# Performance work log

Measured on AMD Instinct MI355X. Metric: run time of the kernel, lower is better.

## Reference

```python
import jax, jax.numpy as jnp
import numpy as np

NIN = 128
NOUT = 128


def setup_inputs() -> dict:
    key = jax.random.key(0)
    k_adj, k_node, k_wi, k_wj = jax.random.split(key, 4)
    B, N = 4, 256
    adj = jax.random.uniform(k_adj, (B, 1, N, N), dtype=jnp.float32)
    node = jax.random.normal(k_node, (B, NIN, N), dtype=jnp.float32)
    # 1x1 conv weights, stored as [nout, nin] (squeezed from [nout, nin, 1, 1])
    scale = 1.0 / np.sqrt(NIN)
    Wi = jax.random.normal(k_wi, (NOUT, NIN), dtype=jnp.float32) * scale
    Wj = jax.random.normal(k_wj, (NOUT, NIN), dtype=jnp.float32) * scale
    return {"adj": adj, "node": node, "Wi": Wi, "Wj": Wj}


def reference(adj, node, Wi, Wj):
    # adj: [B,1,N,N], node: [B,nin,N]
    N = adj.shape[-1]
    # broadcast node across rows and mask by adjacency: [B,nin,N,N]
    x = node[:, :, None, :] * adj
    # 1x1 convs == channel contractions
    yi = jnp.einsum('oc,bcij->boij', Wi, x)
    yj = jnp.einsum('oc,bcij->boij', Wj, x)
    I = jnp.eye(N, dtype=x.dtype)
    return I * yi + (1.0 - I) * yj
```

## Files before the change

kernel.cpp:

```cpp
#include <hip/hip_runtime.h>

#define NIN  128
#define NOUT 128
#define NN   256
#define BB   4

__global__ __launch_bounds__(256) void precompute_u(
    const float* __restrict__ node,
    const float* __restrict__ Wi,
    const float* __restrict__ Wj,
    float* __restrict__ ui,
    float* __restrict__ uj)
{
    const int bo = blockIdx.x;
    const int b  = bo >> 7;
    const int o  = bo & (NOUT - 1);
    const int t  = threadIdx.x;

    const float* np_ = node + (size_t)b * NIN * NN + t;
    const float* wi  = Wi + o * NIN;
    const float* wj  = Wj + o * NIN;

    float ai = 0.f, aj = 0.f;
    #pragma unroll 16
    for (int c = 0; c < NIN; ++c) {
        const float n = np_[c * NN];
        ai = fmaf(wi[c], n, ai);
        aj = fmaf(wj[c], n, aj);
    }
    ui[bo * NN + t] = ai;
    uj[bo * NN + t] = aj;
}

__global__ __launch_bounds__(256) void stream_out(
    const float* __restrict__ adj,
    const float* __restrict__ ui,
    const float* __restrict__ uj,
    float* __restrict__ out)
{
    const int blk = blockIdx.x;
    const int bo  = blk >> 3;
    const int rc  = blk & 7;
    const int b   = bo >> 7;
    const int t   = threadIdx.x;
    const int jb  = (t & 63) << 2;
    const int rr  = t >> 6;

    const float4 vj   = *(const float4*)&uj[bo * NN + jb];
    const float* uip  = ui + bo * NN;
    const float* adjb = adj + (size_t)b * (NN * NN);
    float*       outp = out + (size_t)bo * (NN * NN);

    const int i0 = (rc << 5) + rr;
    #pragma unroll
    for (int r = 0; r < 8; ++r) {
        const int i = i0 + (r << 2);
        const float s_ii = uip[i];
        const float4 a = *(const float4*)&adjb[i * NN + jb];
        float4 v;
        v.x = (i == jb + 0) ? s_ii : vj.x;
        v.y = (i == jb + 1) ? s_ii : vj.y;
        v.z = (i == jb + 2) ? s_ii : vj.z;
        v.w = (i == jb + 3) ? s_ii : vj.w;
        float4 rs;
        rs.x = a.x * v.x;
        rs.y = a.y * v.y;
        rs.z = a.z * v.z;
        rs.w = a.w * v.w;
        *(float4*)&outp[i * NN + jb] = rs;
    }
}

__global__ __launch_bounds__(256) void nodeconv_fused(
    const float* __restrict__ adj, const float* __restrict__ node,
    const float* __restrict__ Wi, const float* __restrict__ Wj,
    float* __restrict__ out)
{
    __shared__ float si[NN];
    __shared__ float sj[NN];
    const int bo = blockIdx.x;
    const int b  = bo >> 7;
    const int o  = bo & (NOUT - 1);
    const int t  = threadIdx.x;
    {
        const float* np_ = node + (size_t)(b * NIN) * NN + t;
        const float* wi  = Wi + o * NIN;
        const float* wj  = Wj + o * NIN;
        float ai = 0.f, aj = 0.f;
        #pragma unroll 8
        for (int c = 0; c < NIN; ++c) {
            const float n = np_[(size_t)c * NN];
            ai += wi[c] * n;
            aj += wj[c] * n;
        }
        si[t] = ai;
        sj[t] = aj;
    }
    __syncthreads();
    const int jb   = (t & 63) << 2;
    const int rrow = t >> 6;
    const float4 vj = *(const float4*)&sj[jb];
    const float* adjb = adj + (size_t)b * (NN * NN);
    float*       outp = out + (size_t)bo * (NN * NN);
    #pragma unroll 4
    for (int r = 0; r < 64; ++r) {
        const int i = (r << 2) + rrow;
        const float s_ii = si[i];
        const float4 a = *(const float4*)&adjb[i * NN + jb];
        float4 v;
        v.x = (i == jb + 0) ? s_ii : vj.x;
        v.y = (i == jb + 1) ? s_ii : vj.y;
        v.z = (i == jb + 2) ? s_ii : vj.z;
        v.w = (i == jb + 3) ? s_ii : vj.w;
        float4 rs;
        rs.x = a.x * v.x; rs.y = a.y * v.y; rs.z = a.z * v.z; rs.w = a.w * v.w;
        *(float4*)&outp[i * NN + jb] = rs;
    }
}

extern "C" void kernel_launch(void* const* d_in, const int* in_sizes, int n_in,
                              void* d_out, int out_size, void* d_ws, size_t ws_size,
                              hipStream_t stream) {
    const float* adj  = (const float*)d_in[0];
    const float* node = (const float*)d_in[1];
    const float* Wi   = (const float*)d_in[2];
    const float* Wj   = (const float*)d_in[3];
    float* out = (float*)d_out;

    const size_t u_elems = (size_t)BB * NOUT * NN;
    const size_t need    = 2 * u_elems * sizeof(float);

    if (ws_size >= need) {
        float* ui = (float*)d_ws;
        float* uj = ui + u_elems;
        precompute_u<<<dim3(BB * NOUT), dim3(256), 0, stream>>>(node, Wi, Wj, ui, uj);
        stream_out<<<dim3(BB * NOUT * 8), dim3(256), 0, stream>>>(adj, ui, uj, out);
    } else {
        nodeconv_fused<<<dim3(BB * NOUT), dim3(256), 0, stream>>>(adj, node, Wi, Wj, out);
    }
}
```

Measured before the change: 147.9 us.

## Reuse adjacency tile across output-channel group and use nontemporal stores

The streaming kernel now loads a 16-row adjacency tile into registers once and reuses it for 8 output channels, instead of reloading adj for every output channel. Stores switch to nontemporal builtins so the large output write stream bypasses cache retention. This cuts adjacency read traffic, which was mostly served by L2 anyway. The cost is fewer blocks (1024 vs 4096), each doing more work, and a different block-to-memory mapping.

```diff
diff --git a/kernel.cpp b/kernel.cpp
--- a/kernel.cpp
+++ b/kernel.cpp
@@ -4,6 +4,8 @@
 #define NOUT 128
 #define NN   256
 #define BB   4
+
+typedef float v4f __attribute__((ext_vector_type(4)));
 
 __global__ __launch_bounds__(256) void precompute_u(
     const float* __restrict__ node,
@@ -32,42 +34,54 @@
     uj[bo * NN + t] = aj;
 }
 
-__global__ __launch_bounds__(256) void stream_out(
+#define OG 8
+#define RCH 16
+
+__global__ __launch_bounds__(256) void stream_out_og(
     const float* __restrict__ adj,
     const float* __restrict__ ui,
     const float* __restrict__ uj,
     float* __restrict__ out)
 {
     const int blk = blockIdx.x;
-    const int bo  = blk >> 3;
-    const int rc  = blk & 7;
-    const int b   = bo >> 7;
-    const int t   = threadIdx.x;
-    const int jb  = (t & 63) << 2;
-    const int rr  = t >> 6;
+    const int og  = blk & 15;
+    const int rc  = (blk >> 4) & 15;
+    const int b   = blk >> 8;
 
-    const float4 vj   = *(const float4*)&uj[bo * NN + jb];
-    const float* uip  = ui + bo * NN;
+    const int t  = threadIdx.x;
+    const int jb = (t & 63) << 2;
+    const int rr = t >> 6;
+
     const float* adjb = adj + (size_t)b * (NN * NN);
-    float*       outp = out + (size_t)bo * (NN * NN);
 
-    const int i0 = (rc << 5) + rr;
+    v4f a[4];
     #pragma unroll
-    for (int r = 0; r < 8; ++r) {
-        const int i = i0 + (r << 2);
-        const float s_ii = uip[i];
-        const float4 a = *(const float4*)&adjb[i * NN + jb];
-        float4 v;
-        v.x = (i == jb + 0) ? s_ii : vj.x;
-        v.y = (i == jb + 1) ? s_ii : vj.y;
-        v.z = (i == jb + 2) ? s_ii : vj.z;
-        v.w = (i == jb + 3) ? s_ii : vj.w;
-        float4 rs;
-        rs.x = a.x * v.x;
-        rs.y = a.y * v.y;
-        rs.z = a.z * v.z;
-        rs.w = a.w * v.w;
-        *(float4*)&outp[i * NN + jb] = rs;
+    for (int r = 0; r < 4; ++r) {
+        const int i = (rc << 4) + rr + (r << 2);
+        a[r] = *(const v4f*)&adjb[i * NN + jb];
+    }
+
+    const int obase = b * NOUT + og * OG;
+
+    #pragma unroll 2
+    for (int o = 0; o < OG; ++o) {
+        const int bo = obase + o;
+        const v4f   vj  = *(const v4f*)&uj[bo * NN + jb];
+        const float* uip = ui + bo * NN;
+        float*       outp = out + (size_t)bo * (NN * NN);
+
+        #pragma unroll
+        for (int r = 0; r < 4; ++r) {
+            const int i = (rc << 4) + rr + (r << 2);
+            const float s_ii = uip[i];
+            v4f v;
+            v.x = (i == jb + 0) ? s_ii : vj.x;
+            v.y = (i == jb + 1) ? s_ii : vj.y;
+            v.z = (i == jb + 2) ? s_ii : vj.z;
+            v.w = (i == jb + 3) ? s_ii : vj.w;
+            const v4f rs = a[r] * v;
+            __builtin_nontemporal_store(rs, (v4f*)&outp[i * NN + jb]);
+        }
     }
 }
 
@@ -134,7 +148,7 @@
         float* ui = (float*)d_ws;
         float* uj = ui + u_elems;
         precompute_u<<<dim3(BB * NOUT), dim3(256), 0, stream>>>(node, Wi, Wj, ui, uj);
-        stream_out<<<dim3(BB * NOUT * 8), dim3(256), 0, stream>>>(adj, ui, uj, out);
+        stream_out_og<<<dim3(BB * (NOUT / OG) * (NN / RCH)), dim3(256), 0, stream>>>(adj, ui, uj, out);
     } else {
         nodeconv_fused<<<dim3(BB * NOUT), dim3(256), 0, stream>>>(adj, node, Wi, Wj, out);
     }
```

After: 152.0 us. 2.8% more time.

## Fuse projection and streaming into one kernel with row chunks and nontemporal stores

Applied to the files above, without the earlier changes.

Replaces the two-kernel path (precompute projections into workspace, then stream output) with a single kernel. Each block recomputes the per-(batch, out-channel) projections into shared memory and then writes a quarter of the output rows, using nontemporal vector stores. This removes the workspace round trip and the second launch. In exchange, the channel contraction is done four times redundantly, once per row chunk.

```diff
diff --git a/kernel.cpp b/kernel.cpp
--- a/kernel.cpp
+++ b/kernel.cpp
@@ -5,116 +5,63 @@
 #define NN   256
 #define BB   4
 
-__global__ __launch_bounds__(256) void precompute_u(
+typedef float v4f __attribute__((ext_vector_type(4)));
+
+#define RCHUNK 64
+
+__global__ __launch_bounds__(256) void nodeconv_fused2(
+    const float* __restrict__ adj,
     const float* __restrict__ node,
     const float* __restrict__ Wi,
     const float* __restrict__ Wj,
-    float* __restrict__ ui,
-    float* __restrict__ uj)
-{
-    const int bo = blockIdx.x;
-    const int b  = bo >> 7;
-    const int o  = bo & (NOUT - 1);
-    const int t  = threadIdx.x;
-
-    const float* np_ = node + (size_t)b * NIN * NN + t;
-    const float* wi  = Wi + o * NIN;
-    const float* wj  = Wj + o * NIN;
-
-    float ai = 0.f, aj = 0.f;
-    #pragma unroll 16
-    for (int c = 0; c < NIN; ++c) {
-        const float n = np_[c * NN];
-        ai = fmaf(wi[c], n, ai);
-        aj = fmaf(wj[c], n, aj);
-    }
-    ui[bo * NN + t] = ai;
-    uj[bo * NN + t] = aj;
-}
-
-__global__ __launch_bounds__(256) void stream_out(
-    const float* __restrict__ adj,
-    const float* __restrict__ ui,
-    const float* __restrict__ uj,
-    float* __restrict__ out)
-{
-    const int blk = blockIdx.x;
-    const int bo  = blk >> 3;
-    const int rc  = blk & 7;
-    const int b   = bo >> 7;
-    const int t   = threadIdx.x;
-    const int jb  = (t & 63) << 2;
-    const int rr  = t >> 6;
-
-    const float4 vj   = *(const float4*)&uj[bo * NN + jb];
-    const float* uip  = ui + bo * NN;
-    const float* adjb = adj + (size_t)b * (NN * NN);
-    float*       outp = out + (size_t)bo * (NN * NN);
-
-    const int i0 = (rc << 5) + rr;
-    #pragma unroll
-    for (int r = 0; r < 8; ++r) {
-        const int i = i0 + (r << 2);
-        const float s_ii = uip[i];
-        const float4 a = *(const float4*)&adjb[i * NN + jb];
-        float4 v;
-        v.x = (i == jb + 0) ? s_ii : vj.x;
-        v.y = (i == jb + 1) ? s_ii : vj.y;
-        v.z = (i == jb + 2) ? s_ii : vj.z;
-        v.w = (i == jb + 3) ? s_ii : vj.w;
-        float4 rs;
-        rs.x = a.x * v.x;
-        rs.y = a.y * v.y;
-        rs.z = a.z * v.z;
-        rs.w = a.w * v.w;
-        *(float4*)&outp[i * NN + jb] = rs;
-    }
-}
-
-__global__ __launch_bounds__(256) void nodeconv_fused(
-    const float* __restrict__ adj, const float* __restrict__ node,
-    const float* __restrict__ Wi, const float* __restrict__ Wj,
     float* __restrict__ out)
 {
     __shared__ float si[NN];
     __shared__ float sj[NN];
-    const int bo = blockIdx.x;
-    const int b  = bo >> 7;
-    const int o  = bo & (NOUT - 1);
-    const int t  = threadIdx.x;
+
+    const int blk = blockIdx.x;
+    const int bo  = blk >> 2;
+    const int rc  = blk & 3;
+    const int b   = bo >> 7;
+    const int o   = bo & (NOUT - 1);
+    const int t   = threadIdx.x;
+
     {
-        const float* np_ = node + (size_t)(b * NIN) * NN + t;
+        const float* np_ = node + (size_t)b * NIN * NN + t;
         const float* wi  = Wi + o * NIN;
         const float* wj  = Wj + o * NIN;
         float ai = 0.f, aj = 0.f;
-        #pragma unroll 8
+        #pragma unroll 16
         for (int c = 0; c < NIN; ++c) {
-            const float n = np_[(size_t)c * NN];
-            ai += wi[c] * n;
-            aj += wj[c] * n;
+            const float n = np_[c * NN];
+            ai = fmaf(wi[c], n, ai);
+            aj = fmaf(wj[c], n, aj);
         }
         si[t] = ai;
         sj[t] = aj;
     }
     __syncthreads();
-    const int jb   = (t & 63) << 2;
-    const int rrow = t >> 6;
-    const float4 vj = *(const float4*)&sj[jb];
+
+    const int jb = (t & 63) << 2;
+    const int rr = t >> 6;
+
+    const v4f vj = *(const v4f*)&sj[jb];
     const float* adjb = adj + (size_t)b * (NN * NN);
     float*       outp = out + (size_t)bo * (NN * NN);
-    #pragma unroll 4
-    for (int r = 0; r < 64; ++r) {
-        const int i = (r << 2) + rrow;
+
+    const int ibase = (rc << 6) + rr;
+    #pragma unroll 8
+    for (int r = 0; r < 16; ++r) {
+        const int i = ibase + (r << 2);
         const float s_ii = si[i];
-        const float4 a = *(const float4*)&adjb[i * NN + jb];
-        float4 v;
+        const v4f a = *(const v4f*)&adjb[i * NN + jb];
+        v4f v;
         v.x = (i == jb + 0) ? s_ii : vj.x;
         v.y = (i == jb + 1) ? s_ii : vj.y;
         v.z = (i == jb + 2) ? s_ii : vj.z;
         v.w = (i == jb + 3) ? s_ii : vj.w;
-        float4 rs;
-        rs.x = a.x * v.x; rs.y = a.y * v.y; rs.z = a.z * v.z; rs.w = a.w * v.w;
-        *(float4*)&outp[i * NN + jb] = rs;
+        const v4f rs = a * v;
+        __builtin_nontemporal_store(rs, (v4f*)&outp[i * NN + jb]);
     }
 }
 
@@ -127,15 +74,8 @@
     const float* Wj   = (const float*)d_in[3];
     float* out = (float*)d_out;
 
-    const size_t u_elems = (size_t)BB * NOUT * NN;
-    const size_t need    = 2 * u_elems * sizeof(float);
+    (void)d_ws; (void)ws_size;
 
-    if (ws_size >= need) {
-        float* ui = (float*)d_ws;
-        float* uj = ui + u_elems;
-        precompute_u<<<dim3(BB * NOUT), dim3(256), 0, stream>>>(node, Wi, Wj, ui, uj);
-        stream_out<<<dim3(BB * NOUT * 8), dim3(256), 0, stream>>>(adj, ui, uj, out);
-    } else {
-        nodeconv_fused<<<dim3(BB * NOUT), dim3(256), 0, stream>>>(adj, node, Wi, Wj, out);
-    }
+    nodeconv_fused2<<<dim3(BB * NOUT * (NN / RCHUNK)), dim3(256), 0, stream>>>(
+        adj, node, Wi, Wj, out);
 }
```

Result: slower. 162.0 us (+9.5%).
